# Performance work log

Measured on AMD Instinct MI355X. Metric: run time of the kernel, lower is better.

Reference implementation:

```python
import jax, jax.numpy as jnp
import numpy as np

NF = 64      # feature channels
DG = 8       # deformable groups
B, H, W = 4, 128, 128
K = 3        # kernel size
TAPS = K * K # 9 sampling taps per pixel per group


def _conv(x, w, b):
    # 3x3 stride-1 SAME conv, NCHW / OIHW
    y = jax.lax.conv_general_dilated(x, w, (1, 1), 'SAME',
                                     dimension_numbers=('NCHW', 'OIHW', 'NCHW'))
    return y + b[None, :, None, None]


def _lrelu(x):
    return jnp.where(x >= 0, x, 0.1 * x)


def _deform_conv(x, off_y, off_x, mask, w, b):
    """Modulated deformable conv v2 (3x3, stride 1, pad 1, dilation 1).
    x:     [B, C, H, W]
    off_y/off_x/mask: [B, dg, 9, H, W]
    w:     [Cout, C, 3, 3], b: [Cout]
    """
    Bn, C, Hn, Wn = x.shape
    dg = off_y.shape[1]
    cg = C // dg
    k = jnp.arange(K, dtype=x.dtype) - (K - 1) / 2  # [-1, 0, 1]
    ky = jnp.repeat(k, K)  # [9] row offsets
    kx = jnp.tile(k, K)    # [9] col offsets
    base_y = jnp.arange(Hn, dtype=x.dtype)[:, None]   # [H,1]
    base_x = jnp.arange(Wn, dtype=x.dtype)[None, :]   # [1,W]
    sy = off_y + ky[None, None, :, None, None] + base_y  # [B,dg,9,H,W]
    sx = off_x + kx[None, None, :, None, None] + base_x
    y0 = jnp.floor(sy)
    x0 = jnp.floor(sx)
    xg = x.reshape(Bn, dg, cg, Hn * Wn)
    val = jnp.zeros((Bn, dg, cg, TAPS, Hn, Wn), x.dtype)
    # bilinear interpolation over 4 corners, zero outside image
    for di in (0.0, 1.0):
        for dj in (0.0, 1.0):
            yi = y0 + di
            xi = x0 + dj
            wgt = (1.0 - jnp.abs(sy - yi)) * (1.0 - jnp.abs(sx - xi))
            valid = (yi >= 0) & (yi < Hn) & (xi >= 0) & (xi < Wn)
            idx = (jnp.clip(yi, 0, Hn - 1).astype(jnp.int32) * Wn
                   + jnp.clip(xi, 0, Wn - 1).astype(jnp.int32))  # [B,dg,9,H,W]
            g = jnp.take_along_axis(
                xg, idx.reshape(Bn, dg, 1, TAPS * Hn * Wn), axis=-1
            ).reshape(Bn, dg, cg, TAPS, Hn, Wn)
            val = val + (wgt * valid.astype(x.dtype))[:, :, None] * g
    val = val * mask[:, :, None]  # modulation
    out = jnp.einsum('bgckhw,ogck->bohw', val,
                     w.reshape(w.shape[0], dg, cg, TAPS))
    return out + b[None, :, None, None]


def setup_inputs() -> dict:
    key = jax.random.key(0)
    ks = jax.random.split(key, 12)
    s = lambda fan: 1.0 / np.sqrt(fan)
    return {
        'nbr': jax.random.normal(ks[0], (B, NF, H, W), jnp.float32),
        'ref': jax.random.normal(ks[1], (B, NF, H, W), jnp.float32),
        'w_off1': jax.random.normal(ks[2], (NF, 2 * NF, K, K), jnp.float32) * s(2 * NF * 9),
        'b_off1': jnp.zeros((NF,), jnp.float32),
        'w_off2': jax.random.normal(ks[3], (NF, NF, K, K), jnp.float32) * s(NF * 9),
        'b_off2': jnp.zeros((NF,), jnp.float32),
        # offset/mask conv: small init keeps sampled offsets modest (as trained DCNs do)
        'w_om': jax.random.normal(ks[4], (3 * DG * TAPS, NF, K, K), jnp.float32) * 0.01,
        'b_om': jnp.zeros((3 * DG * TAPS,), jnp.float32),
        'w_dcn': jax.random.normal(ks[5], (NF, NF, K, K), jnp.float32) * s(NF * 9),
        'b_dcn': jnp.zeros((NF,), jnp.float32),
    }


def reference(nbr, ref, w_off1, b_off1, w_off2, b_off2, w_om, b_om, w_dcn, b_dcn):
    off = _lrelu(_conv(jnp.concatenate([nbr, ref], axis=1), w_off1, b_off1))
    off = _lrelu(_conv(off, w_off2, b_off2))
    om = _conv(off, w_om, b_om)                 # [B, 3*dg*9, H, W]
    o1, o2, m = jnp.split(om, 3, axis=1)        # each [B, dg*9, H, W]
    Bn, _, Hn, Wn = nbr.shape
    off_y = o1.reshape(Bn, DG, TAPS, Hn, Wn)
    off_x = o2.reshape(Bn, DG, TAPS, Hn, Wn)
    mask = jax.nn.sigmoid(m).reshape(Bn, DG, TAPS, Hn, Wn)
    fea = _deform_conv(nbr, off_y, off_x, mask, w_dcn, b_dcn)
    return fea
```

## Files before the change

### kernel.cpp

```cpp
#include <hip/hip_runtime.h>
#include <hip/hip_bf16.h>
#include <math.h>

#define H_DIM 128
#define W_DIM 128
#define BATCH 4
#define HW (H_DIM * W_DIM)

typedef __attribute__((ext_vector_type(8))) short bf16x8;
typedef __attribute__((ext_vector_type(4))) float f32x4;
typedef __attribute__((ext_vector_type(4))) unsigned int u32x4;

static __device__ __forceinline__ unsigned short f2bf(float f) {
    __hip_bfloat16 h = __float2bfloat16(f);
    return *reinterpret_cast<unsigned short*>(&h);
}
static __device__ __forceinline__ float bf2f(unsigned short u) {
    return __uint_as_float(((unsigned int)u) << 16);
}

__global__ __launch_bounds__(256)
void prep_nhwc_kernel(const float* __restrict__ nbr, const float* __restrict__ ref,
                      unsigned short* __restrict__ dst,
                      unsigned short* __restrict__ gmaj) {
    __shared__ float s[128][65];
    const int b  = blockIdx.y;
    const int p0 = blockIdx.x * 64;
    const int t  = threadIdx.x;
    const int px = t & 63;
#pragma unroll
    for (int it = 0; it < 32; ++it) {
        int c = it * 4 + (t >> 6);
        const float* src = (c < 64) ? nbr : ref;
        int cs = c & 63;
        s[c][px] = src[(size_t)(b * 64 + cs) * HW + p0 + px];
    }
    __syncthreads();
#pragma unroll
    for (int it = 0; it < 4; ++it) {
        int idx = it * 256 + t;
        int p  = idx >> 4;
        int ut = idx & 15;
        int x  = (p0 + p) & 127;
        int key = (x + 1) & 7;
        int cpos = (ut & 8) | ((ut & 7) ^ key);
        bf16x8 v;
#pragma unroll
        for (int j = 0; j < 8; ++j)
            v[j] = (short)f2bf(s[ut * 8 + j][p]);
        *(bf16x8*)(dst + ((size_t)(b * HW + p0 + p) * 128 + cpos * 8)) = v;
    }
#pragma unroll
    for (int it = 0; it < 2; ++it) {
        int idx = it * 256 + t;
        int g   = idx >> 6;
        int p2  = idx & 63;
        bf16x8 v;
#pragma unroll
        for (int j = 0; j < 8; ++j)
            v[j] = (short)f2bf(s[g * 8 + j][p2]);
        *(bf16x8*)(gmaj + ((size_t)(b * 8 + g) * HW + p0 + p2) * 8) = v;
    }
}

__global__ void pack_w_kernel(const float* __restrict__ w, unsigned short* __restrict__ dst,
                              int COUT_real, int CIN, int NCF, int NKS) {
    int idx = blockIdx.x * 256 + threadIdx.x;
    int total = NKS * NCF * 64 * 8;
    if (idx >= total) return;
    int j    = idx & 7;
    int lane = (idx >> 3) & 63;
    int frag = idx >> 9;
    int cf   = frag % NCF;
    int ks   = frag / NCF;
    int co = cf * 16 + (lane & 15);
    int k  = ks * 32 + (lane >> 4) * 8 + j;
    int t  = k / CIN;
    int ci = k % CIN;
    float v = (co < COUT_real) ? w[((size_t)co * CIN + ci) * 9 + t] : 0.f;
    dst[idx] = f2bf(v);
}

template<int CIN, int NKS, bool RELU>
__global__ __launch_bounds__(256, 3)
void conv64_mfma_kernel(const unsigned short* __restrict__ in,
                        const unsigned short* __restrict__ wpk,
                        const float* __restrict__ bias,
                        unsigned short* __restrict__ out)
{
    constexpr int ROWB = 66 * CIN * 2;
    __shared__ __align__(16) char smem[3 * ROWB];

    const int rb   = blockIdx.x;
    const int x0   = (rb & 1) * 64;
    const int y    = (rb >> 1) & 127;
    const int b    = rb >> 8;
    const int tid  = threadIdx.x;
    const int lane = tid & 63;
    const int wave = tid >> 6;
    const int l15  = lane & 15;
    const int q    = lane >> 4;
    const u32x4 zv = {0u, 0u, 0u, 0u};

    const int lstart = (x0 == 0) ? 1 : 0;
    const int lzero  = (x0 == 0) ? 0 : 65;
    for (int dy = 0; dy < 3; ++dy) {
        int yy = y + dy - 1;
        char* dstrow = smem + dy * ROWB;
        if (yy >= 0 && yy < H_DIM) {
            const char* src = (const char*)(in +
                ((size_t)(b * H_DIM + yy) * W_DIM + (x0 - 1 + lstart)) * CIN);
            for (int i = tid * 16; i < 65 * CIN * 2; i += 256 * 16)
                *(u32x4*)(dstrow + lstart * CIN * 2 + i) = *(const u32x4*)(src + i);
            if (tid < CIN / 8)
                *(u32x4*)(dstrow + lzero * CIN * 2 + tid * 16) = zv;
        } else {
            for (int i = tid * 16; i < 66 * CIN * 2; i += 256 * 16)
                *(u32x4*)(dstrow + i) = zv;
        }
    }
    __syncthreads();

    f32x4 acc[4];
#pragma unroll
    for (int pf = 0; pf < 4; ++pf)
        acc[pf] = (f32x4){0.f, 0.f, 0.f, 0.f};

#pragma unroll
    for (int ks = 0; ks < NKS; ++ks) {
        const int t   = ks / (CIN / 32);
        const int ci0 = (ks % (CIN / 32)) * 32;
        const int dy = t / 3, dx = t % 3;
        const int u  = (ci0 >> 3) + q;
        bf16x8 a[4];
#pragma unroll
        for (int pf = 0; pf < 4; ++pf) {
            const int l = pf * 16 + l15 + dx;
            const int upos = u ^ (l & 7);
            a[pf] = *(const bf16x8*)(smem + dy * ROWB + (l * CIN + upos * 8) * 2);
        }
        bf16x8 wfr = *(const bf16x8*)(wpk + ((size_t)(ks * 4 + wave) * 64 + lane) * 8);
#pragma unroll
        for (int pf = 0; pf < 4; ++pf)
            acc[pf] = __builtin_amdgcn_mfma_f32_16x16x32_bf16(a[pf], wfr, acc[pf], 0, 0, 0);
    }

    const int co = wave * 16 + l15;
    const float bv = bias[co];
#pragma unroll
    for (int pf = 0; pf < 4; ++pf)
#pragma unroll
        for (int r = 0; r < 4; ++r) {
            int x = x0 + pf * 16 + q * 4 + r;
            float v = acc[pf][r] + bv;
            if (RELU) v = (v >= 0.f) ? v : 0.1f * v;
            int cpos = (((co >> 3) ^ ((x + 1) & 7)) << 3) | (co & 7);
            out[((size_t)(b * H_DIM + y) * W_DIM + x) * 64 + cpos] = f2bf(v);
        }
}

__global__ __launch_bounds__(256, 4)
void conv3om_kernel(const unsigned short* __restrict__ in,
                    const unsigned short* __restrict__ wpk3,
                    const float* __restrict__ bom,
                    unsigned short* __restrict__ omg)
{
    constexpr int ROWB = 66 * 128;
    __shared__ __align__(16) char smem[216 * 72 * 2];
    unsigned short* om_lds = (unsigned short*)smem;

    const int rb   = blockIdx.x;
    const int x0   = (rb & 1) * 64;
    const int y    = (rb >> 1) & 127;
    const int b    = rb >> 8;
    const int tid  = threadIdx.x;
    const int lane = tid & 63;
    const int wave = tid >> 6;
    const int l15  = lane & 15;
    const int q    = lane >> 4;
    const u32x4 zv = {0u, 0u, 0u, 0u};

    const int lstart = (x0 == 0) ? 1 : 0;
    const int lzero  = (x0 == 0) ? 0 : 65;
    for (int dy = 0; dy < 3; ++dy) {
        int yy = y + dy - 1;
        char* dstrow = smem + dy * ROWB;
        if (yy >= 0 && yy < H_DIM) {
            const char* src = (const char*)(in +
                ((size_t)(b * H_DIM + yy) * W_DIM + (x0 - 1 + lstart)) * 64);
            for (int i = tid * 16; i < 65 * 128; i += 256 * 16)
                *(u32x4*)(dstrow + lstart * 128 + i) = *(const u32x4*)(src + i);
            if (tid < 8)
                *(u32x4*)(dstrow + lzero * 128 + tid * 16) = zv;
        } else {
            for (int i = tid * 16; i < 66 * 128; i += 256 * 16)
                *(u32x4*)(dstrow + i) = zv;
        }
    }
    __syncthreads();

    f32x4 acc[4][4];
#pragma unroll
    for (int pf = 0; pf < 4; ++pf)
#pragma unroll
        for (int cfi = 0; cfi < 4; ++cfi)
            acc[pf][cfi] = (f32x4){0.f, 0.f, 0.f, 0.f};

#pragma unroll
    for (int ks = 0; ks < 18; ++ks) {
        const int t   = ks >> 1;
        const int ci0 = (ks & 1) * 32;
        const int dy = t / 3, dx = t % 3;
        bf16x8 a[4];
#pragma unroll
        for (int pf = 0; pf < 4; ++pf) {
            const int l = pf * 16 + l15 + dx;
            const int upos = ((ci0 >> 3) + q) ^ (l & 7);
            a[pf] = *(const bf16x8*)(smem + dy * ROWB + (l * 64 + upos * 8) * 2);
        }
#pragma unroll
        for (int cfi = 0; cfi < 4; ++cfi) {
            const int cf = wave + cfi * 4;
            if (cfi < 3 || wave < 2) {
                bf16x8 wfr = *(const bf16x8*)(wpk3 + ((size_t)(ks * 14 + cf) * 64 + lane) * 8);
#pragma unroll
                for (int pf = 0; pf < 4; ++pf)
                    acc[pf][cfi] = __builtin_amdgcn_mfma_f32_16x16x32_bf16(
                        a[pf], wfr, acc[pf][cfi], 0, 0, 0);
            }
        }
    }
    __syncthreads();

#pragma unroll
    for (int cfi = 0; cfi < 4; ++cfi) {
        const int cf = wave + cfi * 4;
        if (cfi < 3 || wave < 2) {
            const int co = cf * 16 + l15;
            const float bv = (co < 216) ? bom[co] : 0.f;
            if (co < 216) {
#pragma unroll
                for (int pf = 0; pf < 4; ++pf)
#pragma unroll
                    for (int r = 0; r < 4; ++r) {
                        int xl = pf * 16 + q * 4 + r;
                        om_lds[co * 72 + xl] = f2bf(acc[pf][cfi][r] + bv);
                    }
            }
        }
    }
    __syncthreads();

    unsigned short* dst = omg + (size_t)b * 216 * HW + y * W_DIM + x0;
    for (int i = tid; i < 216 * 8; i += 256) {
        int row = i >> 3;
        int seg = i & 7;
        u32x4 v = *(const u32x4*)(om_lds + row * 72 + seg * 8);
        *(u32x4*)(dst + (size_t)row * HW + seg * 8) = v;
    }
}

struct GSlot {
    bf16x8 c00, c01, c10, c11;
    float w00, w01, w10, w11;
};

__global__ __launch_bounds__(256, 4)
void deform_mfma_kernel(const unsigned short* __restrict__ xg,
                        const unsigned short* __restrict__ omg,
                        const unsigned short* __restrict__ wpkD,
                        const float* __restrict__ bdcn,
                        float* __restrict__ out)
{
    const int hwid = blockIdx.x;
    const int rb   = (hwid & 7) * (BATCH * H_DIM * 2 / 8) + (hwid >> 3);

    const int x0   = (rb & 1) * 64;
    const int y    = (rb >> 1) & 127;
    const int b    = rb >> 8;
    const int tid  = threadIdx.x;
    const int lane = tid & 63;
    const int wave = tid >> 6;
    const int l15  = lane & 15;
    const int q    = lane >> 4;
    const int px0w = wave * 16;

    const unsigned short* omb = omg + (size_t)b * 216 * HW;
    const int x   = x0 + px0w + l15;
    const int pix = y * W_DIM + x;

    f32x4 acc2[4];
#pragma unroll
    for (int cf = 0; cf < 4; ++cf)
        acc2[cf] = (f32x4){0.f, 0.f, 0.f, 0.f};

    auto OMLOAD = [&](int ks, float& oy, float& ox, float& mr) {
        const int och = ((ks & 1) * 4 + q) * 9 + (ks >> 1);
        oy = bf2f(__builtin_nontemporal_load(omb + (size_t)och * HW + pix));
        ox = bf2f(__builtin_nontemporal_load(omb + (size_t)(72 + och) * HW + pix));
        mr = bf2f(__builtin_nontemporal_load(omb + (size_t)(144 + och) * HW + pix));
    };

    auto GPREP = [&](int ks, float oy, float ox, float mr, GSlot& s) {
        const int tap = ks >> 1;
        const int g   = (ks & 1) * 4 + q;
        const int dy  = tap / 3 - 1;
        const int dx  = tap % 3 - 1;
        const float mask = 1.f / (1.f + __expf(-mr));

        const float sy = oy + (float)(dy + y);
        const float sx = ox + (float)(dx + x);
        const float fy = floorf(sy);
        const float fx = floorf(sx);
        const int y0  = (int)fy;
        const int xq0 = (int)fx;
        const float ay = sy - fy;
        const float ax = sx - fx;

        const bool vy0 = (y0 >= 0) && (y0 < H_DIM);
        const bool vy1 = (y0 >= -1) && (y0 < H_DIM - 1);
        const bool vx0 = (xq0 >= 0) && (xq0 < W_DIM);
        const bool vx1 = (xq0 >= -1) && (xq0 < W_DIM - 1);

        float w00 = (1.f - ay) * (1.f - ax); if (!(vy0 && vx0)) w00 = 0.f;
        float w01 = (1.f - ay) * ax;         if (!(vy0 && vx1)) w01 = 0.f;
        float w10 = ay * (1.f - ax);         if (!(vy1 && vx0)) w10 = 0.f;
        float w11 = ay * ax;                 if (!(vy1 && vx1)) w11 = 0.f;
        s.w00 = w00 * mask; s.w01 = w01 * mask;
        s.w10 = w10 * mask; s.w11 = w11 * mask;

        const int iy0 = min(max(y0, 0), H_DIM - 1);
        const int iy1 = min(max(y0 + 1, 0), H_DIM - 1);
        const int ix0 = min(max(xq0, 0), W_DIM - 1);
        const int ix1 = min(max(xq0 + 1, 0), W_DIM - 1);

        const unsigned short* gb = xg + (size_t)(b * 8 + g) * HW * 8;
        s.c00 = *(const bf16x8*)(gb + (size_t)(iy0 * W_DIM + ix0) * 8);
        s.c01 = *(const bf16x8*)(gb + (size_t)(iy0 * W_DIM + ix1) * 8);
        s.c10 = *(const bf16x8*)(gb + (size_t)(iy1 * W_DIM + ix0) * 8);
        s.c11 = *(const bf16x8*)(gb + (size_t)(iy1 * W_DIM + ix1) * 8);
    };

    auto CONSUME = [&](int ks, GSlot& s) {
        bf16x8 av;
#pragma unroll
        for (int j = 0; j < 8; ++j) {
            float v = s.w00 * bf2f((unsigned short)s.c00[j])
                    + s.w01 * bf2f((unsigned short)s.c01[j])
                    + s.w10 * bf2f((unsigned short)s.c10[j])
                    + s.w11 * bf2f((unsigned short)s.c11[j]);
            av[j] = (short)f2bf(v);
        }
#pragma unroll
        for (int cf = 0; cf < 4; ++cf) {
            bf16x8 wfr = *(const bf16x8*)(wpkD + ((size_t)(ks * 4 + cf) * 64 + lane) * 8);
            acc2[cf] = __builtin_amdgcn_mfma_f32_16x16x32_bf16(av, wfr, acc2[cf], 0, 0, 0);
        }
    };

    float oyA, oxA, mrA, oyB, oxB, mrB;
    GSlot GA, GB;
    OMLOAD(0, oyA, oxA, mrA);
    OMLOAD(1, oyB, oxB, mrB);
    GPREP(0, oyA, oxA, mrA, GA);
#pragma unroll
    for (int ks = 0; ks < 18; ks += 2) {
        if (ks + 2 < 18) OMLOAD(ks + 2, oyA, oxA, mrA);
        GPREP(ks + 1, oyB, oxB, mrB, GB);
        CONSUME(ks, GA);
        if (ks + 3 < 18) OMLOAD(ks + 3, oyB, oxB, mrB);
        if (ks + 2 < 18) GPREP(ks + 2, oyA, oxA, mrA, GA);
        CONSUME(ks + 1, GB);
    }

#pragma unroll
    for (int cf = 0; cf < 4; ++cf) {
        const int co = cf * 16 + l15;
        const float bv = bdcn[co];
#pragma unroll
        for (int r = 0; r < 4; ++r) {
            int xs = x0 + px0w + q * 4 + r;
            __builtin_nontemporal_store(acc2[cf][r] + bv,
                out + (size_t)(b * 64 + co) * HW + y * W_DIM + xs);
        }
    }
}

extern "C" void kernel_launch(void* const* d_in, const int* in_sizes, int n_in,
                              void* d_out, int out_size, void* d_ws, size_t ws_size,
                              hipStream_t stream) {
    const float* nbr  = (const float*)d_in[0];
    const float* ref  = (const float*)d_in[1];
    const float* w1   = (const float*)d_in[2];
    const float* b1   = (const float*)d_in[3];
    const float* w2   = (const float*)d_in[4];
    const float* b2   = (const float*)d_in[5];
    const float* wom  = (const float*)d_in[6];
    const float* bom  = (const float*)d_in[7];
    const float* wdcn = (const float*)d_in[8];
    const float* bdcn = (const float*)d_in[9];
    float* out = (float*)d_out;
    char* W = (char*)d_ws;

    unsigned short* in1  = (unsigned short*)(W + 0);
    unsigned short* c1o  = (unsigned short*)(W + 16777216);
    unsigned short* c2o  = (unsigned short*)(W + 25165824);
    unsigned short* nbrg = (unsigned short*)(W + 33554432);
    unsigned short* omg  = (unsigned short*)(W + 41943040);
    unsigned short* wpk1 = (unsigned short*)(W + 70254592);
    unsigned short* wpk2 = (unsigned short*)(W + 70402048);
    unsigned short* wpk3 = (unsigned short*)(W + 70475776);
    unsigned short* wpkD = (unsigned short*)(W + 70733824);

    prep_nhwc_kernel<<<dim3(HW / 64, BATCH), 256, 0, stream>>>(nbr, ref, in1, nbrg);
    pack_w_kernel<<<288, 256, 0, stream>>>(w1, wpk1, 64, 128, 4, 36);
    pack_w_kernel<<<144, 256, 0, stream>>>(w2, wpk2, 64, 64, 4, 18);
    pack_w_kernel<<<504, 256, 0, stream>>>(wom, wpk3, 216, 64, 14, 18);
    pack_w_kernel<<<144, 256, 0, stream>>>(wdcn, wpkD, 64, 64, 4, 18);

    conv64_mfma_kernel<128, 36, true>
        <<<dim3(BATCH * H_DIM * 2), 256, 0, stream>>>(in1, wpk1, b1, c1o);
    conv64_mfma_kernel<64, 18, true>
        <<<dim3(BATCH * H_DIM * 2), 256, 0, stream>>>(c1o, wpk2, b2, c2o);

    conv3om_kernel<<<dim3(BATCH * H_DIM * 2), 256, 0, stream>>>(
        c2o, wpk3, bom, omg);
    deform_mfma_kernel<<<dim3(BATCH * H_DIM * 2), 256, 0, stream>>>(
        nbrg, omg, wpkD, bdcn, out);
}
```

Measured before the change: 121.8 us.

## Fuse offset/mask conv into deformable conv kernel and merge weight packing launches

Merges the offset/mask convolution and the deformable sampling conv into one kernel. The 216-channel offset/mask tile stays in LDS instead of being written to global memory and read back, which removes a full-resolution intermediate round trip and one launch. The four weight-pack launches become a single kernel that dispatches on index range. In exchange the fused kernel is larger, its occupancy bound drops from 4 to 3 blocks, and the convolution phase and the sampling phase no longer overlap across separate kernels.

```diff
diff --git a/kernel.cpp b/kernel.cpp
--- a/kernel.cpp
+++ b/kernel.cpp
@@ -63,11 +63,18 @@
     }
 }
 
-__global__ void pack_w_kernel(const float* __restrict__ w, unsigned short* __restrict__ dst,
-                              int COUT_real, int CIN, int NCF, int NKS) {
+__global__ void pack_all_kernel(const float* __restrict__ w1, const float* __restrict__ w2,
+                                const float* __restrict__ wom, const float* __restrict__ wdcn,
+                                unsigned short* __restrict__ wpk1, unsigned short* __restrict__ wpk2,
+                                unsigned short* __restrict__ wpk3, unsigned short* __restrict__ wpkD) {
     int idx = blockIdx.x * 256 + threadIdx.x;
-    int total = NKS * NCF * 64 * 8;
-    if (idx >= total) return;
+    const int N1 = 73728, N2 = 36864, N3 = 129024, N4 = 36864;
+    const float* w; unsigned short* dst; int CIN, NCF, COUT;
+    if (idx < N1)                { w = w1;   dst = wpk1; CIN = 128; NCF = 4;  COUT = 64; }
+    else if (idx < N1+N2)        { idx -= N1;       w = w2;   dst = wpk2; CIN = 64; NCF = 4;  COUT = 64; }
+    else if (idx < N1+N2+N3)     { idx -= N1+N2;    w = wom;  dst = wpk3; CIN = 64; NCF = 14; COUT = 216; }
+    else if (idx < N1+N2+N3+N4)  { idx -= N1+N2+N3; w = wdcn; dst = wpkD; CIN = 64; NCF = 4;  COUT = 64; }
+    else return;
     int j    = idx & 7;
     int lane = (idx >> 3) & 63;
     int frag = idx >> 9;
@@ -77,7 +84,7 @@
     int k  = ks * 32 + (lane >> 4) * 8 + j;
     int t  = k / CIN;
     int ci = k % CIN;
-    float v = (co < COUT_real) ? w[((size_t)co * CIN + ci) * 9 + t] : 0.f;
+    float v = (co < COUT) ? w[((size_t)co * CIN + ci) * 9 + t] : 0.f;
     dst[idx] = f2bf(v);
 }
 
@@ -159,17 +166,26 @@
         }
 }
 
-__global__ __launch_bounds__(256, 4)
-void conv3om_kernel(const unsigned short* __restrict__ in,
-                    const unsigned short* __restrict__ wpk3,
-                    const float* __restrict__ bom,
-                    unsigned short* __restrict__ omg)
+struct GSlot {
+    bf16x8 c00, c01, c10, c11;
+    float w00, w01, w10, w11;
+};
+
+__global__ __launch_bounds__(256, 3)
+void fused_om_deform_kernel(const unsigned short* __restrict__ in,
+                            const unsigned short* __restrict__ xg,
+                            const unsigned short* __restrict__ wpk3,
+                            const unsigned short* __restrict__ wpkD,
+                            const float* __restrict__ bom,
+                            const float* __restrict__ bdcn,
+                            float* __restrict__ out)
 {
     constexpr int ROWB = 66 * 128;
     __shared__ __align__(16) char smem[216 * 72 * 2];
     unsigned short* om_lds = (unsigned short*)smem;
 
-    const int rb   = blockIdx.x;
+    const int hwid = blockIdx.x;
+    const int rb   = (hwid & 7) * (BATCH * H_DIM * 2 / 8) + (hwid >> 3);
     const int x0   = (rb & 1) * 64;
     const int y    = (rb >> 1) & 127;
     const int b    = rb >> 8;
@@ -199,95 +215,63 @@
     }
     __syncthreads();
 
-    f32x4 acc[4][4];
-#pragma unroll
-    for (int pf = 0; pf < 4; ++pf)
-#pragma unroll
-        for (int cfi = 0; cfi < 4; ++cfi)
-            acc[pf][cfi] = (f32x4){0.f, 0.f, 0.f, 0.f};
-
-#pragma unroll
-    for (int ks = 0; ks < 18; ++ks) {
-        const int t   = ks >> 1;
-        const int ci0 = (ks & 1) * 32;
-        const int dy = t / 3, dx = t % 3;
-        bf16x8 a[4];
-#pragma unroll
-        for (int pf = 0; pf < 4; ++pf) {
-            const int l = pf * 16 + l15 + dx;
-            const int upos = ((ci0 >> 3) + q) ^ (l & 7);
-            a[pf] = *(const bf16x8*)(smem + dy * ROWB + (l * 64 + upos * 8) * 2);
-        }
+    {
+        f32x4 acc[4][4];
+#pragma unroll
+        for (int pf = 0; pf < 4; ++pf)
+#pragma unroll
+            for (int cfi = 0; cfi < 4; ++cfi)
+                acc[pf][cfi] = (f32x4){0.f, 0.f, 0.f, 0.f};
+
+#pragma unroll
+        for (int ks = 0; ks < 18; ++ks) {
+            const int t   = ks >> 1;
+            const int ci0 = (ks & 1) * 32;
+            const int dy = t / 3, dx = t % 3;
+            bf16x8 a[4];
+#pragma unroll
+            for (int pf = 0; pf < 4; ++pf) {
+                const int l = pf * 16 + l15 + dx;
+                const int upos = ((ci0 >> 3) + q) ^ (l & 7);
+                a[pf] = *(const bf16x8*)(smem + dy * ROWB + (l * 64 + upos * 8) * 2);
+            }
+#pragma unroll
+            for (int cfi = 0; cfi < 4; ++cfi) {
+                const int cf = wave + cfi * 4;
+                if (cfi < 3 || wave < 2) {
+                    bf16x8 wfr = *(const bf16x8*)(wpk3 + ((size_t)(ks * 14 + cf) * 64 + lane) * 8);
+#pragma unroll
+                    for (int pf = 0; pf < 4; ++pf)
+                        acc[pf][cfi] = __builtin_amdgcn_mfma_f32_16x16x32_bf16(
+                            a[pf], wfr, acc[pf][cfi], 0, 0, 0);
+                }
+            }
+        }
+        __syncthreads();
+
 #pragma unroll
         for (int cfi = 0; cfi < 4; ++cfi) {
             const int cf = wave + cfi * 4;
             if (cfi < 3 || wave < 2) {
-                bf16x8 wfr = *(const bf16x8*)(wpk3 + ((size_t)(ks * 14 + cf) * 64 + lane) * 8);
-#pragma unroll
-                for (int pf = 0; pf < 4; ++pf)
-                    acc[pf][cfi] = __builtin_amdgcn_mfma_f32_16x16x32_bf16(
-                        a[pf], wfr, acc[pf][cfi], 0, 0, 0);
+                const int co = cf * 16 + l15;
+                if (co < 216) {
+                    const float bv = bom[co];
+#pragma unroll
+                    for (int pf = 0; pf < 4; ++pf)
+#pragma unroll
+                        for (int r = 0; r < 4; ++r) {
+                            int xl = pf * 16 + q * 4 + r;
+                            om_lds[co * 72 + xl] = f2bf(acc[pf][cfi][r] + bv);
+                        }
+                }
             }
         }
     }
     __syncthreads();
 
-#pragma unroll
-    for (int cfi = 0; cfi < 4; ++cfi) {
-        const int cf = wave + cfi * 4;
-        if (cfi < 3 || wave < 2) {
-            const int co = cf * 16 + l15;
-            const float bv = (co < 216) ? bom[co] : 0.f;
-            if (co < 216) {
-#pragma unroll
-                for (int pf = 0; pf < 4; ++pf)
-#pragma unroll
-                    for (int r = 0; r < 4; ++r) {
-                        int xl = pf * 16 + q * 4 + r;
-                        om_lds[co * 72 + xl] = f2bf(acc[pf][cfi][r] + bv);
-                    }
-            }
-        }
-    }
-    __syncthreads();
-
-    unsigned short* dst = omg + (size_t)b * 216 * HW + y * W_DIM + x0;
-    for (int i = tid; i < 216 * 8; i += 256) {
-        int row = i >> 3;
-        int seg = i & 7;
-        u32x4 v = *(const u32x4*)(om_lds + row * 72 + seg * 8);
-        *(u32x4*)(dst + (size_t)row * HW + seg * 8) = v;
-    }
-}
-
-struct GSlot {
-    bf16x8 c00, c01, c10, c11;
-    float w00, w01, w10, w11;
-};
-
-__global__ __launch_bounds__(256, 4)
-void deform_mfma_kernel(const unsigned short* __restrict__ xg,
-                        const unsigned short* __restrict__ omg,
-                        const unsigned short* __restrict__ wpkD,
-                        const float* __restrict__ bdcn,
-                        float* __restrict__ out)
-{
-    const int hwid = blockIdx.x;
-    const int rb   = (hwid & 7) * (BATCH * H_DIM * 2 / 8) + (hwid >> 3);
-
-    const int x0   = (rb & 1) * 64;
-    const int y    = (rb >> 1) & 127;
-    const int b    = rb >> 8;
-    const int tid  = threadIdx.x;
-    const int lane = tid & 63;
-    const int wave = tid >> 6;
-    const int l15  = lane & 15;
-    const int q    = lane >> 4;
     const int px0w = wave * 16;
-
-    const unsigned short* omb = omg + (size_t)b * 216 * HW;
-    const int x   = x0 + px0w + l15;
-    const int pix = y * W_DIM + x;
+    const int x    = x0 + px0w + l15;
+    const int xl   = px0w + l15;
 
     f32x4 acc2[4];
 #pragma unroll
@@ -296,9 +280,9 @@
 
     auto OMLOAD = [&](int ks, float& oy, float& ox, float& mr) {
         const int och = ((ks & 1) * 4 + q) * 9 + (ks >> 1);
-        oy = bf2f(__builtin_nontemporal_load(omb + (size_t)och * HW + pix));
-        ox = bf2f(__builtin_nontemporal_load(omb + (size_t)(72 + och) * HW + pix));
-        mr = bf2f(__builtin_nontemporal_load(omb + (size_t)(144 + och) * HW + pix));
+        oy = bf2f(om_lds[och * 72 + xl]);
+        ox = bf2f(om_lds[(72 + och) * 72 + xl]);
+        mr = bf2f(om_lds[(144 + och) * 72 + xl]);
     };
 
     auto GPREP = [&](int ks, float oy, float ox, float mr, GSlot& s) {
@@ -406,25 +390,20 @@
     unsigned short* c1o  = (unsigned short*)(W + 16777216);
     unsigned short* c2o  = (unsigned short*)(W + 25165824);
     unsigned short* nbrg = (unsigned short*)(W + 33554432);
-    unsigned short* omg  = (unsigned short*)(W + 41943040);
-    unsigned short* wpk1 = (unsigned short*)(W + 70254592);
-    unsigned short* wpk2 = (unsigned short*)(W + 70402048);
-    unsigned short* wpk3 = (unsigned short*)(W + 70475776);
-    unsigned short* wpkD = (unsigned short*)(W + 70733824);
+    unsigned short* wpk1 = (unsigned short*)(W + 41943040);
+    unsigned short* wpk2 = (unsigned short*)(W + 42090496);
+    unsigned short* wpk3 = (unsigned short*)(W + 42164224);
+    unsigned short* wpkD = (unsigned short*)(W + 42422272);
 
     prep_nhwc_kernel<<<dim3(HW / 64, BATCH), 256, 0, stream>>>(nbr, ref, in1, nbrg);
-    pack_w_kernel<<<288, 256, 0, stream>>>(w1, wpk1, 64, 128, 4, 36);
-    pack_w_kernel<<<144, 256, 0, stream>>>(w2, wpk2, 64, 64, 4, 18);
-    pack_w_kernel<<<504, 256, 0, stream>>>(wom, wpk3, 216, 64, 14, 18);
-    pack_w_kernel<<<144, 256, 0, stream>>>(wdcn, wpkD, 64, 64, 4, 18);
+    pack_all_kernel<<<1080, 256, 0, stream>>>(w1, w2, wom, wdcn,
+                                              wpk1, wpk2, wpk3, wpkD);
 
     conv64_mfma_kernel<128, 36, true>
         <<<dim3(BATCH * H_DIM * 2), 256, 0, stream>>>(in1, wpk1, b1, c1o);
     conv64_mfma_kernel<64, 18, true>
         <<<dim3(BATCH * H_DIM * 2), 256, 0, stream>>>(c1o, wpk2, b2, c2o);
 
-    conv3om_kernel<<<dim3(BATCH * H_DIM * 2), 256, 0, stream>>>(
-        c2o, wpk3, bom, omg);
-    deform_mfma_kernel<<<dim3(BATCH * H_DIM * 2), 256, 0, stream>>>(
-        nbrg, omg, wpkD, bdcn, out);
-}
+    fused_om_deform_kernel<<<dim3(BATCH * H_DIM * 2), 256, 0, stream>>>(
+        c2o, nbrg, wpk3, wpkD, bom, bdcn, out);
+}
```

After: 100.0 us. 1.22x faster.

## Use packed fp16 bilinear interpolation and f16 MFMA in deformable conv, merge weight packs

Applied to the files above, without the earlier changes.

Stores the group-major neighbor features and the deformable-conv weights as fp16 instead of bf16. The bilinear gather-blend then runs as packed half2 FMAs and feeds an f16 MFMA, removing the per-element bf16-to-float unpack and float-to-bf16 repack. It also merges the four weight-packing launches into one kernel to cut launch overhead. The risks are fp16 range and precision for features and interpolation weights, and loss of the float accumulation inside the blend.

```diff
diff --git a/kernel.cpp b/kernel.cpp
--- a/kernel.cpp
+++ b/kernel.cpp
@@ -8,8 +8,11 @@
 #define HW (H_DIM * W_DIM)
 
 typedef __attribute__((ext_vector_type(8))) short bf16x8;
+typedef __attribute__((ext_vector_type(4))) short s16x4;
 typedef __attribute__((ext_vector_type(4))) float f32x4;
 typedef __attribute__((ext_vector_type(4))) unsigned int u32x4;
+typedef _Float16 f16x2 __attribute__((ext_vector_type(2)));
+typedef _Float16 f16x8 __attribute__((ext_vector_type(8)));
 
 static __device__ __forceinline__ unsigned short f2bf(float f) {
     __hip_bfloat16 h = __float2bfloat16(f);
@@ -17,6 +20,10 @@
 }
 static __device__ __forceinline__ float bf2f(unsigned short u) {
     return __uint_as_float(((unsigned int)u) << 16);
+}
+static __device__ __forceinline__ unsigned short f2h(float f) {
+    _Float16 h = (_Float16)f;
+    return *reinterpret_cast<unsigned short*>(&h);
 }
 
 __global__ __launch_bounds__(256)
@@ -58,16 +65,23 @@
         bf16x8 v;
 #pragma unroll
         for (int j = 0; j < 8; ++j)
-            v[j] = (short)f2bf(s[g * 8 + j][p2]);
+            v[j] = (short)f2h(s[g * 8 + j][p2]);
         *(bf16x8*)(gmaj + ((size_t)(b * 8 + g) * HW + p0 + p2) * 8) = v;
     }
 }
 
-__global__ void pack_w_kernel(const float* __restrict__ w, unsigned short* __restrict__ dst,
-                              int COUT_real, int CIN, int NCF, int NKS) {
+__global__ void pack_all_kernel(const float* __restrict__ w1, const float* __restrict__ w2,
+                                const float* __restrict__ wom, const float* __restrict__ wdcn,
+                                unsigned short* __restrict__ wpk1, unsigned short* __restrict__ wpk2,
+                                unsigned short* __restrict__ wpk3, unsigned short* __restrict__ wpkD) {
     int idx = blockIdx.x * 256 + threadIdx.x;
-    int total = NKS * NCF * 64 * 8;
-    if (idx >= total) return;
+    const int N1 = 73728, N2 = 36864, N3 = 129024, N4 = 36864;
+    const float* w; unsigned short* dst; int CIN, NCF, COUT; bool asF16 = false;
+    if (idx < N1)                { w = w1;   dst = wpk1; CIN = 128; NCF = 4;  COUT = 64; }
+    else if (idx < N1+N2)        { idx -= N1;       w = w2;   dst = wpk2; CIN = 64; NCF = 4;  COUT = 64; }
+    else if (idx < N1+N2+N3)     { idx -= N1+N2;    w = wom;  dst = wpk3; CIN = 64; NCF = 14; COUT = 216; }
+    else if (idx < N1+N2+N3+N4)  { idx -= N1+N2+N3; w = wdcn; dst = wpkD; CIN = 64; NCF = 4;  COUT = 64; asF16 = true; }
+    else return;
     int j    = idx & 7;
     int lane = (idx >> 3) & 63;
     int frag = idx >> 9;
@@ -77,8 +91,8 @@
     int k  = ks * 32 + (lane >> 4) * 8 + j;
     int t  = k / CIN;
     int ci = k % CIN;
-    float v = (co < COUT_real) ? w[((size_t)co * CIN + ci) * 9 + t] : 0.f;
-    dst[idx] = f2bf(v);
+    float v = (co < COUT) ? w[((size_t)co * CIN + ci) * 9 + t] : 0.f;
+    dst[idx] = asF16 ? f2h(v) : f2bf(v);
 }
 
 template<int CIN, int NKS, bool RELU>
@@ -237,8 +251,8 @@
         const int cf = wave + cfi * 4;
         if (cfi < 3 || wave < 2) {
             const int co = cf * 16 + l15;
-            const float bv = (co < 216) ? bom[co] : 0.f;
             if (co < 216) {
+                const float bv = bom[co];
 #pragma unroll
                 for (int pf = 0; pf < 4; ++pf)
 #pragma unroll
@@ -261,8 +275,8 @@
 }
 
 struct GSlot {
-    bf16x8 c00, c01, c10, c11;
-    float w00, w01, w10, w11;
+    f16x8 c00, c01, c10, c11;
+    f16x2 w00, w01, w10, w11;
 };
 
 __global__ __launch_bounds__(256, 4)
@@ -326,8 +340,11 @@
         float w01 = (1.f - ay) * ax;         if (!(vy0 && vx1)) w01 = 0.f;
         float w10 = ay * (1.f - ax);         if (!(vy1 && vx0)) w10 = 0.f;
         float w11 = ay * ax;                 if (!(vy1 && vx1)) w11 = 0.f;
-        s.w00 = w00 * mask; s.w01 = w01 * mask;
-        s.w10 = w10 * mask; s.w11 = w11 * mask;
+        w00 *= mask; w01 *= mask; w10 *= mask; w11 *= mask;
+        { _Float16 h = (_Float16)w00; s.w00 = (f16x2){h, h}; }
+        { _Float16 h = (_Float16)w01; s.w01 = (f16x2){h, h}; }
+        { _Float16 h = (_Float16)w10; s.w10 = (f16x2){h, h}; }
+        { _Float16 h = (_Float16)w11; s.w11 = (f16x2){h, h}; }
 
         const int iy0 = min(max(y0, 0), H_DIM - 1);
         const int iy1 = min(max(y0 + 1, 0), H_DIM - 1);
@@ -335,42 +352,45 @@
         const int ix1 = min(max(xq0 + 1, 0), W_DIM - 1);
 
         const unsigned short* gb = xg + (size_t)(b * 8 + g) * HW * 8;
-        s.c00 = *(const bf16x8*)(gb + (size_t)(iy0 * W_DIM + ix0) * 8);
-        s.c01 = *(const bf16x8*)(gb + (size_t)(iy0 * W_DIM + ix1) * 8);
-        s.c10 = *(const bf16x8*)(gb + (size_t)(iy1 * W_DIM + ix0) * 8);
-        s.c11 = *(const bf16x8*)(gb + (size_t)(iy1 * W_DIM + ix1) * 8);
+        s.c00 = *(const f16x8*)(gb + (size_t)(iy0 * W_DIM + ix0) * 8);
+        s.c01 = *(const f16x8*)(gb + (size_t)(iy0 * W_DIM + ix1) * 8);
+        s.c10 = *(const f16x8*)(gb + (size_t)(iy1 * W_DIM + ix0) * 8);
+        s.c11 = *(const f16x8*)(gb + (size_t)(iy1 * W_DIM + ix1) * 8);
     };
 
     auto CONSUME = [&](int ks, GSlot& s) {
-        bf16x8 av;
-#pragma unroll
-        for (int j = 0; j < 8; ++j) {
-            float v = s.w00 * bf2f((unsigned short)s.c00[j])
-                    + s.w01 * bf2f((unsigned short)s.c01[j])
-                    + s.w10 * bf2f((unsigned short)s.c10[j])
-                    + s.w11 * bf2f((unsigned short)s.c11[j]);
-            av[j] = (short)f2bf(v);
-        }
+        f16x8 av;
+        const f16x2* c00 = reinterpret_cast<const f16x2*>(&s.c00);
+        const f16x2* c01 = reinterpret_cast<const f16x2*>(&s.c01);
+        const f16x2* c10 = reinterpret_cast<const f16x2*>(&s.c10);
+        const f16x2* c11 = reinterpret_cast<const f16x2*>(&s.c11);
+        f16x2* avp = reinterpret_cast<f16x2*>(&av);
+#pragma unroll
+        for (int j = 0; j < 4; ++j)
+            avp[j] = s.w00 * c00[j] + s.w01 * c01[j]
+                   + s.w10 * c10[j] + s.w11 * c11[j];
 #pragma unroll
         for (int cf = 0; cf < 4; ++cf) {
-            bf16x8 wfr = *(const bf16x8*)(wpkD + ((size_t)(ks * 4 + cf) * 64 + lane) * 8);
-            acc2[cf] = __builtin_amdgcn_mfma_f32_16x16x32_bf16(av, wfr, acc2[cf], 0, 0, 0);
+            f16x8 wfr = *(const f16x8*)(wpkD + ((size_t)(ks * 4 + cf) * 64 + lane) * 8);
+            acc2[cf] = __builtin_amdgcn_mfma_f32_16x16x32_f16(av, wfr, acc2[cf], 0, 0, 0);
         }
     };
 
-    float oyA, oxA, mrA, oyB, oxB, mrB;
-    GSlot GA, GB;
-    OMLOAD(0, oyA, oxA, mrA);
-    OMLOAD(1, oyB, oxB, mrB);
-    GPREP(0, oyA, oxA, mrA, GA);
-#pragma unroll
-    for (int ks = 0; ks < 18; ks += 2) {
-        if (ks + 2 < 18) OMLOAD(ks + 2, oyA, oxA, mrA);
-        GPREP(ks + 1, oyB, oxB, mrB, GB);
-        CONSUME(ks, GA);
-        if (ks + 3 < 18) OMLOAD(ks + 3, oyB, oxB, mrB);
-        if (ks + 2 < 18) GPREP(ks + 2, oyA, oxA, mrA, GA);
-        CONSUME(ks + 1, GB);
+    {
+        float oyA, oxA, mrA, oyB, oxB, mrB;
+        GSlot GA, GB;
+        OMLOAD(0, oyA, oxA, mrA);
+        OMLOAD(1, oyB, oxB, mrB);
+        GPREP(0, oyA, oxA, mrA, GA);
+#pragma unroll
+        for (int ks = 0; ks < 18; ks += 2) {
+            if (ks + 2 < 18) OMLOAD(ks + 2, oyA, oxA, mrA);
+            GPREP(ks + 1, oyB, oxB, mrB, GB);
+            CONSUME(ks, GA);
+            if (ks + 3 < 18) OMLOAD(ks + 3, oyB, oxB, mrB);
+            if (ks + 2 < 18) GPREP(ks + 2, oyA, oxA, mrA, GA);
+            CONSUME(ks + 1, GB);
+        }
     }
 
 #pragma unroll
@@ -413,10 +433,8 @@
     unsigned short* wpkD = (unsigned short*)(W + 70733824);
 
     prep_nhwc_kernel<<<dim3(HW / 64, BATCH), 256, 0, stream>>>(nbr, ref, in1, nbrg);
-    pack_w_kernel<<<288, 256, 0, stream>>>(w1, wpk1, 64, 128, 4, 36);
-    pack_w_kernel<<<144, 256, 0, stream>>>(w2, wpk2, 64, 64, 4, 18);
-    pack_w_kernel<<<504, 256, 0, stream>>>(wom, wpk3, 216, 64, 14, 18);
-    pack_w_kernel<<<144, 256, 0, stream>>>(wdcn, wpkD, 64, 64, 4, 18);
+    pack_all_kernel<<<1080, 256, 0, stream>>>(w1, w2, wom, wdcn,
+                                              wpk1, wpk2, wpk3, wpkD);
 
     conv64_mfma_kernel<128, 36, true>
         <<<dim3(BATCH * H_DIM * 2), 256, 0, stream>>>(in1, wpk1, b1, c1o);
```

Measured after the change: 115.0 us. 5.6% less time.
